# Performance work log

Hardware: AMD Instinct MI355X
Metric: run time of the kernel (lower is better)

## Reference

```python
import jax, jax.numpy as jnp
import numpy as np

N_V = 100000   # vertices
N_E = 20000    # hyperedges
N_PAIRS = 1600000  # incidence pairs
F = 128
H = 128
EPS = 1e-5


def setup_inputs() -> dict:
    key = jax.random.key(0)
    k1, k2, k3, k4 = jax.random.split(key, 4)
    X = jax.random.normal(k1, (N_V, F), dtype=jnp.float32)
    vertex_ids = jax.random.randint(k2, (N_PAIRS,), 0, N_V, dtype=jnp.int32)
    edge_ids = jax.random.randint(k3, (N_PAIRS,), 0, N_E, dtype=jnp.int32)
    W = jax.random.normal(k4, (F, H), dtype=jnp.float32) * (1.0 / np.sqrt(F))
    b = jnp.zeros((H,), dtype=jnp.float32)
    gamma = jnp.ones((H,), dtype=jnp.float32)
    beta = jnp.zeros((H,), dtype=jnp.float32)
    return {"X": X, "vertex_ids": vertex_ids, "edge_ids": edge_ids,
            "W": W, "b": b, "gamma": gamma, "beta": beta}


def _segment_mean(vals, ids, num_segments):
    s = jax.ops.segment_sum(vals, ids, num_segments=num_segments)
    cnt = jax.ops.segment_sum(jnp.ones((ids.shape[0], 1), vals.dtype), ids,
                              num_segments=num_segments)
    return s / jnp.maximum(cnt, 1.0)


def reference(X, vertex_ids, edge_ids, W, b, gamma, beta):
    # linear: theta
    h = X @ W + b                                    # [N_V, H]
    # batchnorm (batch statistics, as in training mode)
    mu = jnp.mean(h, axis=0)
    var = jnp.var(h, axis=0)
    h = (h - mu) * jax.lax.rsqrt(var + EPS) * gamma + beta
    # hypergraph v2v mean: vertex -> hyperedge mean, then hyperedge -> vertex mean
    Xe = _segment_mean(h[vertex_ids], edge_ids, N_E)   # [N_E, H]
    Xv = _segment_mean(Xe[edge_ids], vertex_ids, N_V)  # [N_V, H]
    # activation (ReLU); dropout is identity in eval
    return jax.nn.relu(Xv)
```

## Files before the change

kernel.cpp:

```cpp
#include <hip/hip_runtime.h>
#include <hip/hip_bf16.h>

#define N_V 100000
#define N_E 20000
#define N_P 1600000
#define FDIM 128
#define HDIM 128
#define BN_EPS 1e-5f

#define SORT_C 4096
#define SORT_BLOCKS ((N_P + SORT_C - 1) / SORT_C)
#define NB_E 313
#define EB_SHIFT 6
#define EB_REGION 9216
#define EB_SORT 5888
#define NB_V 391
#define VB_SHIFT 8
#define VB_REGION 8192
#define VB_SORT 4608
#define SENTINEL 0xFFFFFFFFu

#define EIDX_CAP 192
#define VIDX_CAP 64

typedef __attribute__((ext_vector_type(8))) short short8;
typedef __attribute__((ext_vector_type(4))) float floatx4;

__device__ __forceinline__ float bf_lo(unsigned u) {
    return __uint_as_float(u << 16);
}
__device__ __forceinline__ float bf_hi(unsigned u) {
    return __uint_as_float(u & 0xffff0000u);
}
__device__ __forceinline__ unsigned short f2bf(float f) {
    unsigned u = __float_as_uint(f);
    return (unsigned short)((u + 0x7fffu + ((u >> 16) & 1u)) >> 16);
}

__device__ __forceinline__ void acc4(float* s, const uint2& u) {
    s[0] += bf_lo(u.x); s[1] += bf_hi(u.x);
    s[2] += bf_lo(u.y); s[3] += bf_hi(u.y);
}

__device__ __forceinline__ void acc8(float* s, const uint4& u) {
    s[0] += bf_lo(u.x); s[1] += bf_hi(u.x);
    s[2] += bf_lo(u.y); s[3] += bf_hi(u.y);
    s[4] += bf_lo(u.z); s[5] += bf_hi(u.z);
    s[6] += bf_lo(u.w); s[7] += bf_hi(u.w);
}

#define GEMM_BLOCKS 625
#define WT_STRIDE 136
__global__ __launch_bounds__(256) void k_gemm_mfma(
    const float* __restrict__ X, const float* __restrict__ W,
    const float* __restrict__ bias, unsigned* __restrict__ h_u) {
    __shared__ unsigned short WTs[FDIM * WT_STRIDE];
    const int t = threadIdx.x;
    for (int idx = t; idx < FDIM * HDIM; idx += 256) {
        const int k = idx >> 7, m = idx & 127;
        WTs[m * WT_STRIDE + k] = f2bf(W[idx]);
    }
    __syncthreads();

    const int wave = t >> 6, lane = t & 63;
    const int quad = lane >> 4, sub = lane & 15;
    const int nstrips = N_V / 16;

    for (int s = blockIdx.x * 4 + wave; s < nstrips; s += GEMM_BLOCKS * 4) {
        const int row0 = s * 16;
        short8 xf[4];
        const float* xp = X + (size_t)(row0 + sub) * FDIM + quad * 8;
        #pragma unroll
        for (int kt = 0; kt < 4; ++kt) {
            const float4 a = *(const float4*)(xp + kt * 32);
            const float4 b2 = *(const float4*)(xp + kt * 32 + 4);
            short8 f;
            f[0] = (short)f2bf(a.x);  f[1] = (short)f2bf(a.y);
            f[2] = (short)f2bf(a.z);  f[3] = (short)f2bf(a.w);
            f[4] = (short)f2bf(b2.x); f[5] = (short)f2bf(b2.y);
            f[6] = (short)f2bf(b2.z); f[7] = (short)f2bf(b2.w);
            xf[kt] = f;
        }
        #pragma unroll
        for (int tile = 0; tile < 8; ++tile) {
            floatx4 acc = {0.f, 0.f, 0.f, 0.f};
            const unsigned short* wp =
                WTs + (tile * 16 + sub) * WT_STRIDE + quad * 8;
            #pragma unroll
            for (int kt = 0; kt < 4; ++kt) {
                const short8 af = *(const short8*)(wp + kt * 32);
                acc = __builtin_amdgcn_mfma_f32_16x16x32_bf16(af, xf[kt], acc,
                                                              0, 0, 0);
            }
            const int ch = tile * 16 + quad * 4;
            const float4 bb = *(const float4*)(bias + ch);
            const float c0 = acc[0] + bb.x, c1 = acc[1] + bb.y;
            const float c2 = acc[2] + bb.z, c3 = acc[3] + bb.w;
            const unsigned lo = (unsigned)f2bf(c0) | ((unsigned)f2bf(c1) << 16);
            const unsigned hi = (unsigned)f2bf(c2) | ((unsigned)f2bf(c3) << 16);
            uint2* dst = (uint2*)(h_u + (size_t)(row0 + sub) * 64 + (ch >> 1));
            *dst = make_uint2(lo, hi);
        }
    }
}

#define BN_BLOCKS 400
#define BN_RPB 250
__global__ __launch_bounds__(256) void k_bn_stats(
    const unsigned* __restrict__ h_u, float* __restrict__ sums ) {
    const int t = threadIdx.x;
    const int c8 = t & 15;
    const int rw = t >> 4;
    const int r0 = blockIdx.x * BN_RPB;
    const int r1 = min(r0 + BN_RPB, N_V);
    float s[8] = {0.f,0.f,0.f,0.f,0.f,0.f,0.f,0.f};
    float ss[8] = {0.f,0.f,0.f,0.f,0.f,0.f,0.f,0.f};
    for (int r = r0 + rw; r < r1; r += 16) {
        const uint4 u = *(const uint4*)(h_u + (size_t)r * 64 + c8 * 4);
        const float x0 = bf_lo(u.x), x1 = bf_hi(u.x);
        const float x2 = bf_lo(u.y), x3 = bf_hi(u.y);
        const float x4 = bf_lo(u.z), x5 = bf_hi(u.z);
        const float x6 = bf_lo(u.w), x7 = bf_hi(u.w);
        s[0]+=x0; ss[0]+=x0*x0;  s[1]+=x1; ss[1]+=x1*x1;
        s[2]+=x2; ss[2]+=x2*x2;  s[3]+=x3; ss[3]+=x3*x3;
        s[4]+=x4; ss[4]+=x4*x4;  s[5]+=x5; ss[5]+=x5*x5;
        s[6]+=x6; ss[6]+=x6*x6;  s[7]+=x7; ss[7]+=x7*x7;
    }
    #pragma unroll
    for (int k = 0; k < 8; ++k) {
        s[k]  += __shfl_xor(s[k], 16);  s[k]  += __shfl_xor(s[k], 32);
        ss[k] += __shfl_xor(ss[k], 16); ss[k] += __shfl_xor(ss[k], 32);
    }
    __shared__ float ls[128], lss[128];
    for (int k = t; k < 128; k += 256) { ls[k] = 0.f; lss[k] = 0.f; }
    __syncthreads();
    if ((t & 63) < 16) {
        #pragma unroll
        for (int k = 0; k < 8; ++k) {
            atomicAdd(&ls[c8 * 8 + k], s[k]);
            atomicAdd(&lss[c8 * 8 + k], ss[k]);
        }
    }
    __syncthreads();
    if (t < 128) {
        atomicAdd(&sums[t],       ls[t]);
        atomicAdd(&sums[128 + t], lss[t]);
    }
}

__global__ void k_bn_final(const float* __restrict__ sums,
                           const float* __restrict__ gamma,
                           const float* __restrict__ beta,
                           float* __restrict__ scale, float* __restrict__ shift) {
    const int c = threadIdx.x;
    const float inv_n = 1.0f / (float)N_V;
    const float mu  = sums[c] * inv_n;
    const float var = sums[128 + c] * inv_n - mu * mu;
    const float inv = rsqrtf(var + BN_EPS);
    const float sc  = gamma[c] * inv;
    scale[c] = sc;
    shift[c] = beta[c] - mu * sc;
}

__global__ __launch_bounds__(256) void k_sort_dual(
    const int* __restrict__ vid, const int* __restrict__ eid,
    int* __restrict__ gcntE, int* __restrict__ gcntV,
    unsigned* __restrict__ partE, unsigned* __restrict__ partV) {
    __shared__ unsigned stageE[SORT_C];
    __shared__ unsigned stageV[SORT_C];
    __shared__ int histE[NB_E], curE[NB_E], offsE[NB_E], gbaseE[NB_E];
    __shared__ int histV[NB_V], curV[NB_V], offsV[NB_V], gbaseV[NB_V];
    __shared__ int partial[256];
    const int t = threadIdx.x;
    const int p0 = blockIdx.x * SORT_C;
    const int n = min(SORT_C, N_P - p0);

    for (int k = t; k < NB_E; k += 256) histE[k] = 0;
    for (int k = t; k < NB_V; k += 256) histV[k] = 0;
    __syncthreads();
    for (int i = t; i < n; i += 256) {
        atomicAdd(&histE[((unsigned)eid[p0 + i]) >> EB_SHIFT], 1);
        atomicAdd(&histV[((unsigned)vid[p0 + i]) >> VB_SHIFT], 1);
    }
    __syncthreads();
    {
        constexpr int G = (NB_E + 255) / 256;
        int loc[G]; int s = 0;
        #pragma unroll
        for (int g = 0; g < G; ++g) {
            int idx = t * G + g; loc[g] = s;
            if (idx < NB_E) s += histE[idx];
        }
        partial[t] = s;
        __syncthreads();
        for (int d = 1; d < 256; d <<= 1) {
            int x = (t >= d) ? partial[t - d] : 0;
            __syncthreads(); partial[t] += x; __syncthreads();
        }
        const int base = t ? partial[t - 1] : 0;
        #pragma unroll
        for (int g = 0; g < G; ++g) {
            int idx = t * G + g;
            if (idx < NB_E) { offsE[idx] = base + loc[g]; curE[idx] = base + loc[g]; }
        }
        __syncthreads();
    }
    {
        constexpr int G = (NB_V + 255) / 256;
        int loc[G]; int s = 0;
        #pragma unroll
        for (int g = 0; g < G; ++g) {
            int idx = t * G + g; loc[g] = s;
            if (idx < NB_V) s += histV[idx];
        }
        partial[t] = s;
        __syncthreads();
        for (int d = 1; d < 256; d <<= 1) {
            int x = (t >= d) ? partial[t - d] : 0;
            __syncthreads(); partial[t] += x; __syncthreads();
        }
        const int base = t ? partial[t - 1] : 0;
        #pragma unroll
        for (int g = 0; g < G; ++g) {
            int idx = t * G + g;
            if (idx < NB_V) { offsV[idx] = base + loc[g]; curV[idx] = base + loc[g]; }
        }
        __syncthreads();
    }
    for (int i = t; i < n; i += 256) {
        const int ev = eid[p0 + i], vv = vid[p0 + i];
        const unsigned pkE = ((unsigned)(ev & 63) << 17) | (unsigned)vv;
        stageE[atomicAdd(&curE[(unsigned)ev >> EB_SHIFT], 1)] = pkE;
        const unsigned pkV = ((unsigned)(vv & 255) << 15) | (unsigned)ev;
        stageV[atomicAdd(&curV[(unsigned)vv >> VB_SHIFT], 1)] = pkV;
    }
    __syncthreads();
    for (int k = t; k < NB_E; k += 256) {
        const int c = histE[k];
        gbaseE[k] = c ? atomicAdd(&gcntE[k], (c + 15) & ~15) : 0;
    }
    for (int k = t; k < NB_V; k += 256) {
        const int c = histV[k];
        gbaseV[k] = c ? atomicAdd(&gcntV[k], (c + 15) & ~15) : 0;
    }
    __syncthreads();
    for (int k = t >> 3; k < NB_E; k += 32) {
        const int c = histE[k];
        if (c == 0) continue;
        int cpad = (c + 15) & ~15;
        const int gb = gbaseE[k];
        if (gb >= EB_REGION) continue;
        cpad = min(cpad, EB_REGION - gb);
        unsigned* dst = partE + (size_t)k * EB_REGION + gb;
        const int lo = offsE[k];
        for (int j = t & 7; j < cpad; j += 8)
            dst[j] = (j < c) ? stageE[lo + j] : SENTINEL;
    }
    for (int k = t >> 3; k < NB_V; k += 32) {
        const int c = histV[k];
        if (c == 0) continue;
        int cpad = (c + 15) & ~15;
        const int gb = gbaseV[k];
        if (gb >= VB_REGION) continue;
        cpad = min(cpad, VB_REGION - gb);
        unsigned* dst = partV + (size_t)k * VB_REGION + gb;
        const int lo = offsV[k];
        for (int j = t & 7; j < cpad; j += 8)
            dst[j] = (j < c) ? stageV[lo + j] : SENTINEL;
    }
}

template <int NKEY, int PACK_SHIFT, int CAP, int REGION, int STRIDE>
__global__ __launch_bounds__(256) void k_csr(
    const unsigned* __restrict__ part, const int* __restrict__ gcnt,
    int nkeys_total, int* __restrict__ segoff, int* __restrict__ segcnt,
    unsigned* __restrict__ csr) {
    __shared__ unsigned A[CAP];
    __shared__ unsigned B[CAP];
    __shared__ int hist[NKEY], offs[NKEY + 1], cur[NKEY];
    __shared__ int lcur;
    const int bkt = blockIdx.x;
    const int t = threadIdx.x;
    const int lane = t & 63;
    const unsigned mask = (1u << PACK_SHIFT) - 1u;
    const int tot = min(gcnt[bkt], REGION);
    const unsigned* src = part + (size_t)bkt * REGION;

    if (t == 0) lcur = 0;
    for (int k = t; k < NKEY; k += 256) hist[k] = 0;
    __syncthreads();
    for (int i = t; i < ((tot + 255) & ~255); i += 256) {
        unsigned a = (i < tot) ? src[i] : SENTINEL;
        const bool valid = (a != SENTINEL);
        const unsigned long long bal = __ballot(valid);
        int wbase = 0;
        if (lane == 0) wbase = atomicAdd(&lcur, __popcll(bal));
        wbase = __shfl(wbase, 0);
        if (valid) {
            const int pos = wbase + __popcll(bal & ((1ull << lane) - 1ull));
            if (pos < CAP) A[pos] = a;
        }
    }
    __syncthreads();
    const int total = min(lcur, CAP);
    for (int i = t; i < total; i += 256)
        atomicAdd(&hist[A[i] >> PACK_SHIFT], 1);
    __syncthreads();
    if (t == 0) {
        int acc = 0;
        for (int k = 0; k < NKEY; ++k) { offs[k] = acc; acc += hist[k]; }
        offs[NKEY] = acc;
    }
    for (int k = t; k < NKEY; k += 256) cur[k] = 0;
    __syncthreads();
    for (int i = t; i < total; i += 256) {
        const unsigned a = A[i];
        const int k = a >> PACK_SHIFT;
        const int pos = offs[k] + atomicAdd(&cur[k], 1);
        B[pos] = a & mask;
    }
    __syncthreads();
    unsigned* dst = csr + (size_t)bkt * STRIDE;
    for (int i = t; i < total; i += 256) dst[i] = B[i];
    for (int k = t; k < NKEY; k += 256) {
        const int g = bkt * NKEY + k;
        if (g < nkeys_total) {
            segoff[g] = bkt * STRIDE + offs[k];
            segcnt[g] = hist[k];
        }
    }
}

__global__ __launch_bounds__(256) void k_edge_gather(
    const unsigned* __restrict__ h_u, const unsigned* __restrict__ csrE,
    const int* __restrict__ eoff, const int* __restrict__ ecnt,
    const float* __restrict__ scale, const float* __restrict__ shift,
    unsigned* __restrict__ xe_u) {
    __shared__ int ib[4][EIDX_CAP];
    const int b = blockIdx.x;
    const int xcd = b & 7;
    const int half = xcd >> 2;
    const int grp = (b >> 3) * 4 + (xcd & 3);
    const int wave = threadIdx.x >> 6;
    const int e = grp * 4 + wave;
    const int l = threadIdx.x & 63;
    const int rg = l >> 4, c = l & 15;
    const int wbase = half * 32 + 2 * c;
    int o = 0, n = 0;
    if (e < N_E) { o = eoff[e]; n = ecnt[e]; }
    const int nc = min(n, EIDX_CAP);
    int* mi = ib[wave];
    for (int i = l; i < nc; i += 64) mi[i] = csrE[o + i];
    __syncthreads();

    float s[4] = {0.f, 0.f, 0.f, 0.f};
    int j = 0;
    for (; j + 31 < nc; j += 32) {
        const int r0 = mi[j + rg],      r1 = mi[j + 4 + rg];
        const int r2 = mi[j + 8 + rg],  r3 = mi[j + 12 + rg];
        const int r4 = mi[j + 16 + rg], r5 = mi[j + 20 + rg];
        const int r6 = mi[j + 24 + rg], r7 = mi[j + 28 + rg];
        const uint2 u0 = *(const uint2*)(h_u + (size_t)r0 * 64 + wbase);
        const uint2 u1 = *(const uint2*)(h_u + (size_t)r1 * 64 + wbase);
        const uint2 u2 = *(const uint2*)(h_u + (size_t)r2 * 64 + wbase);
        const uint2 u3 = *(const uint2*)(h_u + (size_t)r3 * 64 + wbase);
        const uint2 u4 = *(const uint2*)(h_u + (size_t)r4 * 64 + wbase);
        const uint2 u5 = *(const uint2*)(h_u + (size_t)r5 * 64 + wbase);
        const uint2 u6 = *(const uint2*)(h_u + (size_t)r6 * 64 + wbase);
        const uint2 u7 = *(const uint2*)(h_u + (size_t)r7 * 64 + wbase);
        acc4(s, u0); acc4(s, u1); acc4(s, u2); acc4(s, u3);
        acc4(s, u4); acc4(s, u5); acc4(s, u6); acc4(s, u7);
    }
    for (; j + 15 < nc; j += 16) {
        const int r0 = mi[j + rg],     r1 = mi[j + 4 + rg];
        const int r2 = mi[j + 8 + rg], r3 = mi[j + 12 + rg];
        const uint2 u0 = *(const uint2*)(h_u + (size_t)r0 * 64 + wbase);
        const uint2 u1 = *(const uint2*)(h_u + (size_t)r1 * 64 + wbase);
        const uint2 u2 = *(const uint2*)(h_u + (size_t)r2 * 64 + wbase);
        const uint2 u3 = *(const uint2*)(h_u + (size_t)r3 * 64 + wbase);
        acc4(s, u0); acc4(s, u1); acc4(s, u2); acc4(s, u3);
    }
    for (; j < nc; j += 4) {
        if (j + rg < nc) {
            const int r = mi[j + rg];
            const uint2 u = *(const uint2*)(h_u + (size_t)r * 64 + wbase);
            acc4(s, u);
        }
    }
    for (int jj = nc; jj < n; jj += 4) {
        if (jj + rg < n) {
            const int r = csrE[o + jj + rg];
            const uint2 u = *(const uint2*)(h_u + (size_t)r * 64 + wbase);
            acc4(s, u);
        }
    }
    #pragma unroll
    for (int k = 0; k < 4; ++k) {
        s[k] += __shfl_xor(s[k], 16);
        s[k] += __shfl_xor(s[k], 32);
    }
    if (e < N_E && rg == 0) {
        float m[4] = {0.f, 0.f, 0.f, 0.f};
        if (n > 0) {
            const float rc = 1.0f / (float)n;
            const float4 sc4 = ((const float4*)scale)[half * 16 + c];
            const float4 sh4 = ((const float4*)shift)[half * 16 + c];
            m[0] = sc4.x * s[0] * rc + sh4.x;
            m[1] = sc4.y * s[1] * rc + sh4.y;
            m[2] = sc4.z * s[2] * rc + sh4.z;
            m[3] = sc4.w * s[3] * rc + sh4.w;
        }
        uint2 pk;
        pk.x = (unsigned)f2bf(m[0]) | ((unsigned)f2bf(m[1]) << 16);
        pk.y = (unsigned)f2bf(m[2]) | ((unsigned)f2bf(m[3]) << 16);
        *(uint2*)(xe_u + (size_t)e * 64 + wbase) = pk;
    }
}

__global__ __launch_bounds__(256) void k_vert_gather(
    const unsigned* __restrict__ xe_u, const unsigned* __restrict__ csrV,
    const int* __restrict__ voff, const int* __restrict__ vcnt,
    float* __restrict__ out) {
    __shared__ int ib[4][VIDX_CAP];
    const int wave = threadIdx.x >> 6;
    const int v = blockIdx.x * 4 + wave;
    const int l = threadIdx.x & 63;
    const int g = l >> 4, c = l & 15;
    int o = 0, n = 0;
    if (v < N_V) { o = voff[v]; n = vcnt[v]; }
    const int nc = min(n, VIDX_CAP);
    int* mi = ib[wave];
    for (int i = l; i < nc; i += 64) mi[i] = csrV[o + i];
    __syncthreads();

    float s[8] = {0.f, 0.f, 0.f, 0.f, 0.f, 0.f, 0.f, 0.f};
    int j = 0;
    for (; j + 15 < nc; j += 16) {
        const int r0 = mi[j + g],     r1 = mi[j + 4 + g];
        const int r2 = mi[j + 8 + g], r3 = mi[j + 12 + g];
        const uint4 u0 = *(const uint4*)(xe_u + (size_t)r0 * 64 + 4 * c);
        const uint4 u1 = *(const uint4*)(xe_u + (size_t)r1 * 64 + 4 * c);
        const uint4 u2 = *(const uint4*)(xe_u + (size_t)r2 * 64 + 4 * c);
        const uint4 u3 = *(const uint4*)(xe_u + (size_t)r3 * 64 + 4 * c);
        acc8(s, u0); acc8(s, u1); acc8(s, u2); acc8(s, u3);
    }
    for (; j < nc; j += 4) {
        if (j + g < nc) {
            const int r = mi[j + g];
            const uint4 u = *(const uint4*)(xe_u + (size_t)r * 64 + 4 * c);
            acc8(s, u);
        }
    }
    for (int jj = nc; jj < n; jj += 4) {
        if (jj + g < n) {
            const int r = csrV[o + jj + g];
            const uint4 u = *(const uint4*)(xe_u + (size_t)r * 64 + 4 * c);
            acc8(s, u);
        }
    }
    #pragma unroll
    for (int k = 0; k < 8; ++k) {
        s[k] += __shfl_xor(s[k], 16);
        s[k] += __shfl_xor(s[k], 32);
    }
    if (v < N_V && g == 0) {
        const float rc = 1.0f / (float)max(n, 1);
        float4 r0, r1;
        r0.x = fmaxf(s[0] * rc, 0.f);
        r0.y = fmaxf(s[1] * rc, 0.f);
        r0.z = fmaxf(s[2] * rc, 0.f);
        r0.w = fmaxf(s[3] * rc, 0.f);
        r1.x = fmaxf(s[4] * rc, 0.f);
        r1.y = fmaxf(s[5] * rc, 0.f);
        r1.z = fmaxf(s[6] * rc, 0.f);
        r1.w = fmaxf(s[7] * rc, 0.f);
        ((float4*)out)[(size_t)v * 32 + 2 * c]     = r0;
        ((float4*)out)[(size_t)v * 32 + 2 * c + 1] = r1;
    }
}

extern "C" void kernel_launch(void* const* d_in, const int* in_sizes, int n_in,
                              void* d_out, int out_size, void* d_ws, size_t ws_size,
                              hipStream_t stream) {
    const float* X     = (const float*)d_in[0];
    const int*   vid   = (const int*)d_in[1];
    const int*   eid   = (const int*)d_in[2];
    const float* W     = (const float*)d_in[3];
    const float* b     = (const float*)d_in[4];
    const float* gamma = (const float*)d_in[5];
    const float* beta  = (const float*)d_in[6];
    float* out = (float*)d_out;

    char* ws = (char*)d_ws;
    unsigned* h_u   = (unsigned*)ws;  ws += (size_t)N_V * 64 * 4;
    unsigned* xe_u  = (unsigned*)ws;  ws += (size_t)N_E * 64 * 4;
    unsigned* partE = (unsigned*)ws;  ws += (size_t)NB_E * EB_REGION * 4;
    unsigned* partV = (unsigned*)ws;  ws += (size_t)NB_V * VB_REGION * 4;
    unsigned* csrE  = (unsigned*)ws;  ws += (size_t)NB_E * EB_SORT * 4;
    unsigned* csrV  = (unsigned*)ws;  ws += (size_t)NB_V * VB_SORT * 4;
    int* eoff = (int*)ws;             ws += (size_t)N_E * 4;
    int* ecnt = (int*)ws;             ws += (size_t)N_E * 4;
    int* voff = (int*)ws;             ws += (size_t)N_V * 4;
    int* vcnt = (int*)ws;             ws += (size_t)N_V * 4;
    char* zbase = ws;
    int*   gcntE = (int*)ws;          ws += (size_t)NB_E * 4;
    int*   gcntV = (int*)ws;          ws += (size_t)NB_V * 4;
    float* sums  = (float*)ws;        ws += 256 * 4;
    float* scale = (float*)ws;        ws += 128 * 4;
    float* shift = (float*)ws;        ws += 128 * 4;

    hipMemsetAsync(zbase, 0, (size_t)((char*)scale - zbase), stream);

    k_gemm_mfma<<<GEMM_BLOCKS, 256, 0, stream>>>(X, W, b, h_u);
    k_bn_stats<<<BN_BLOCKS, 256, 0, stream>>>(h_u, sums);
    k_bn_final<<<1, 128, 0, stream>>>(sums, gamma, beta, scale, shift);

    k_sort_dual<<<SORT_BLOCKS, 256, 0, stream>>>(vid, eid, gcntE, gcntV,
                                                 partE, partV);

    k_csr<64, 17, EB_SORT, EB_REGION, EB_SORT>
        <<<NB_E, 256, 0, stream>>>(partE, gcntE, N_E, eoff, ecnt, csrE);
    k_csr<256, 15, VB_SORT, VB_REGION, VB_SORT>
        <<<NB_V, 256, 0, stream>>>(partV, gcntV, N_V, voff, vcnt, csrV);

    k_edge_gather<<<(N_E / 4) * 2, 256, 0, stream>>>(h_u, csrE, eoff, ecnt,
                                                     scale, shift, xe_u);
    k_vert_gather<<<(N_V + 3) / 4, 256, 0, stream>>>(xe_u, csrV, voff, vcnt,
                                                     out);
}
```

Measured before the change: 310.6 us.

## Replace bucketed two-level sort with global-atomic histogram, scan, and scatter CSR build

The CSR construction used to be a per-block bucket sort into padded regions followed by per-bucket local counting sorts. It is now three simple kernels: a global-atomic histogram over every edge and vertex id, a single-pass scan per key set, and an atomic scatter straight into exact CSR arrays. This removes the padded intermediate buffers, the sentinel compaction and the capacity clamps. In exchange it relies on heavy global atomics and uncoalesced scattered writes, and the order of entries within each segment becomes nondeterministic.

Measured after the change: 778.1 us. 2.51x slower.

```diff
diff --git a/kernel.cpp b/kernel.cpp
--- a/kernel.cpp
+++ b/kernel.cpp
@@ -7,18 +7,6 @@
 #define FDIM 128
 #define HDIM 128
 #define BN_EPS 1e-5f
-
-#define SORT_C 4096
-#define SORT_BLOCKS ((N_P + SORT_C - 1) / SORT_C)
-#define NB_E 313
-#define EB_SHIFT 6
-#define EB_REGION 9216
-#define EB_SORT 5888
-#define NB_V 391
-#define VB_SHIFT 8
-#define VB_REGION 8192
-#define VB_SORT 4608
-#define SENTINEL 0xFFFFFFFFu
 
 #define EIDX_CAP 192
 #define VIDX_CAP 64
@@ -162,177 +150,70 @@
     shift[c] = beta[c] - mu * sc;
 }
 
-__global__ __launch_bounds__(256) void k_sort_dual(
+#define HIST_BLOCKS 1024
+__global__ __launch_bounds__(256) void k_hist(
     const int* __restrict__ vid, const int* __restrict__ eid,
-    int* __restrict__ gcntE, int* __restrict__ gcntV,
-    unsigned* __restrict__ partE, unsigned* __restrict__ partV) {
-    __shared__ unsigned stageE[SORT_C];
-    __shared__ unsigned stageV[SORT_C];
-    __shared__ int histE[NB_E], curE[NB_E], offsE[NB_E], gbaseE[NB_E];
-    __shared__ int histV[NB_V], curV[NB_V], offsV[NB_V], gbaseV[NB_V];
-    __shared__ int partial[256];
+    int* __restrict__ histE, int* __restrict__ histV) {
+    const int tid = blockIdx.x * 256 + threadIdx.x;
+    for (int i = tid; i < N_P / 4; i += HIST_BLOCKS * 256) {
+        const int4 e4 = ((const int4*)eid)[i];
+        const int4 v4 = ((const int4*)vid)[i];
+        atomicAdd(&histE[e4.x], 1); atomicAdd(&histE[e4.y], 1);
+        atomicAdd(&histE[e4.z], 1); atomicAdd(&histE[e4.w], 1);
+        atomicAdd(&histV[v4.x], 1); atomicAdd(&histV[v4.y], 1);
+        atomicAdd(&histV[v4.z], 1); atomicAdd(&histV[v4.w], 1);
+    }
+}
+
+__global__ __launch_bounds__(1024) void k_scan(
+    const int* __restrict__ histE, int* __restrict__ eoff, int* __restrict__ ecnt,
+    const int* __restrict__ histV, int* __restrict__ voff, int* __restrict__ vcnt) {
+    __shared__ int partial[1024];
     const int t = threadIdx.x;
-    const int p0 = blockIdx.x * SORT_C;
-    const int n = min(SORT_C, N_P - p0);
-
-    for (int k = t; k < NB_E; k += 256) histE[k] = 0;
-    for (int k = t; k < NB_V; k += 256) histV[k] = 0;
-    __syncthreads();
-    for (int i = t; i < n; i += 256) {
-        atomicAdd(&histE[((unsigned)eid[p0 + i]) >> EB_SHIFT], 1);
-        atomicAdd(&histV[((unsigned)vid[p0 + i]) >> VB_SHIFT], 1);
-    }
-    __syncthreads();
-    {
-        constexpr int G = (NB_E + 255) / 256;
-        int loc[G]; int s = 0;
-        #pragma unroll
-        for (int g = 0; g < G; ++g) {
-            int idx = t * G + g; loc[g] = s;
-            if (idx < NB_E) s += histE[idx];
-        }
-        partial[t] = s;
-        __syncthreads();
-        for (int d = 1; d < 256; d <<= 1) {
-            int x = (t >= d) ? partial[t - d] : 0;
-            __syncthreads(); partial[t] += x; __syncthreads();
-        }
-        const int base = t ? partial[t - 1] : 0;
-        #pragma unroll
-        for (int g = 0; g < G; ++g) {
-            int idx = t * G + g;
-            if (idx < NB_E) { offsE[idx] = base + loc[g]; curE[idx] = base + loc[g]; }
-        }
-        __syncthreads();
-    }
-    {
-        constexpr int G = (NB_V + 255) / 256;
-        int loc[G]; int s = 0;
-        #pragma unroll
-        for (int g = 0; g < G; ++g) {
-            int idx = t * G + g; loc[g] = s;
-            if (idx < NB_V) s += histV[idx];
-        }
-        partial[t] = s;
-        __syncthreads();
-        for (int d = 1; d < 256; d <<= 1) {
-            int x = (t >= d) ? partial[t - d] : 0;
-            __syncthreads(); partial[t] += x; __syncthreads();
-        }
-        const int base = t ? partial[t - 1] : 0;
-        #pragma unroll
-        for (int g = 0; g < G; ++g) {
-            int idx = t * G + g;
-            if (idx < NB_V) { offsV[idx] = base + loc[g]; curV[idx] = base + loc[g]; }
-        }
-        __syncthreads();
-    }
-    for (int i = t; i < n; i += 256) {
-        const int ev = eid[p0 + i], vv = vid[p0 + i];
-        const unsigned pkE = ((unsigned)(ev & 63) << 17) | (unsigned)vv;
-        stageE[atomicAdd(&curE[(unsigned)ev >> EB_SHIFT], 1)] = pkE;
-        const unsigned pkV = ((unsigned)(vv & 255) << 15) | (unsigned)ev;
-        stageV[atomicAdd(&curV[(unsigned)vv >> VB_SHIFT], 1)] = pkV;
-    }
-    __syncthreads();
-    for (int k = t; k < NB_E; k += 256) {
-        const int c = histE[k];
-        gbaseE[k] = c ? atomicAdd(&gcntE[k], (c + 15) & ~15) : 0;
-    }
-    for (int k = t; k < NB_V; k += 256) {
-        const int c = histV[k];
-        gbaseV[k] = c ? atomicAdd(&gcntV[k], (c + 15) & ~15) : 0;
-    }
-    __syncthreads();
-    for (int k = t >> 3; k < NB_E; k += 32) {
-        const int c = histE[k];
-        if (c == 0) continue;
-        int cpad = (c + 15) & ~15;
-        const int gb = gbaseE[k];
-        if (gb >= EB_REGION) continue;
-        cpad = min(cpad, EB_REGION - gb);
-        unsigned* dst = partE + (size_t)k * EB_REGION + gb;
-        const int lo = offsE[k];
-        for (int j = t & 7; j < cpad; j += 8)
-            dst[j] = (j < c) ? stageE[lo + j] : SENTINEL;
-    }
-    for (int k = t >> 3; k < NB_V; k += 32) {
-        const int c = histV[k];
-        if (c == 0) continue;
-        int cpad = (c + 15) & ~15;
-        const int gb = gbaseV[k];
-        if (gb >= VB_REGION) continue;
-        cpad = min(cpad, VB_REGION - gb);
-        unsigned* dst = partV + (size_t)k * VB_REGION + gb;
-        const int lo = offsV[k];
-        for (int j = t & 7; j < cpad; j += 8)
-            dst[j] = (j < c) ? stageV[lo + j] : SENTINEL;
-    }
-}
-
-template <int NKEY, int PACK_SHIFT, int CAP, int REGION, int STRIDE>
-__global__ __launch_bounds__(256) void k_csr(
-    const unsigned* __restrict__ part, const int* __restrict__ gcnt,
-    int nkeys_total, int* __restrict__ segoff, int* __restrict__ segcnt,
-    unsigned* __restrict__ csr) {
-    __shared__ unsigned A[CAP];
-    __shared__ unsigned B[CAP];
-    __shared__ int hist[NKEY], offs[NKEY + 1], cur[NKEY];
-    __shared__ int lcur;
-    const int bkt = blockIdx.x;
-    const int t = threadIdx.x;
-    const int lane = t & 63;
-    const unsigned mask = (1u << PACK_SHIFT) - 1u;
-    const int tot = min(gcnt[bkt], REGION);
-    const unsigned* src = part + (size_t)bkt * REGION;
-
-    if (t == 0) lcur = 0;
-    for (int k = t; k < NKEY; k += 256) hist[k] = 0;
-    __syncthreads();
-    for (int i = t; i < ((tot + 255) & ~255); i += 256) {
-        unsigned a = (i < tot) ? src[i] : SENTINEL;
-        const bool valid = (a != SENTINEL);
-        const unsigned long long bal = __ballot(valid);
-        int wbase = 0;
-        if (lane == 0) wbase = atomicAdd(&lcur, __popcll(bal));
-        wbase = __shfl(wbase, 0);
-        if (valid) {
-            const int pos = wbase + __popcll(bal & ((1ull << lane) - 1ull));
-            if (pos < CAP) A[pos] = a;
-        }
-    }
-    __syncthreads();
-    const int total = min(lcur, CAP);
-    for (int i = t; i < total; i += 256)
-        atomicAdd(&hist[A[i] >> PACK_SHIFT], 1);
-    __syncthreads();
-    if (t == 0) {
-        int acc = 0;
-        for (int k = 0; k < NKEY; ++k) { offs[k] = acc; acc += hist[k]; }
-        offs[NKEY] = acc;
-    }
-    for (int k = t; k < NKEY; k += 256) cur[k] = 0;
-    __syncthreads();
-    for (int i = t; i < total; i += 256) {
-        const unsigned a = A[i];
-        const int k = a >> PACK_SHIFT;
-        const int pos = offs[k] + atomicAdd(&cur[k], 1);
-        B[pos] = a & mask;
-    }
-    __syncthreads();
-    unsigned* dst = csr + (size_t)bkt * STRIDE;
-    for (int i = t; i < total; i += 256) dst[i] = B[i];
-    for (int k = t; k < NKEY; k += 256) {
-        const int g = bkt * NKEY + k;
-        if (g < nkeys_total) {
-            segoff[g] = bkt * STRIDE + offs[k];
-            segcnt[g] = hist[k];
-        }
+    const int* hist; int* off; int* cnt; int n;
+    if (blockIdx.x == 0) { hist = histE; off = eoff; cnt = ecnt; n = N_E; }
+    else                 { hist = histV; off = voff; cnt = vcnt; n = N_V; }
+    const int chunk = (n + 1023) / 1024;
+    const int lo = t * chunk, hi = min(lo + chunk, n);
+    int s = 0;
+    for (int i = lo; i < hi; ++i) s += hist[i];
+    partial[t] = s;
+    __syncthreads();
+    for (int d = 1; d < 1024; d <<= 1) {
+        int x = (t >= d) ? partial[t - d] : 0;
+        __syncthreads(); partial[t] += x; __syncthreads();
+    }
+    int base = t ? partial[t - 1] : 0;
+    for (int i = lo; i < hi; ++i) {
+        const int h = hist[i];
+        off[i] = base; cnt[i] = h; base += h;
+    }
+}
+
+#define SCAT_BLOCKS 1024
+__global__ __launch_bounds__(256) void k_scatter(
+    const int* __restrict__ vid, const int* __restrict__ eid,
+    const int* __restrict__ eoff, const int* __restrict__ voff,
+    int* __restrict__ curE, int* __restrict__ curV,
+    int* __restrict__ csrE, int* __restrict__ csrV) {
+    const int tid = blockIdx.x * 256 + threadIdx.x;
+    for (int i = tid; i < N_P / 4; i += SCAT_BLOCKS * 256) {
+        const int4 e4 = ((const int4*)eid)[i];
+        const int4 v4 = ((const int4*)vid)[i];
+        int p;
+        p = atomicAdd(&curE[e4.x], 1); csrE[eoff[e4.x] + p] = v4.x;
+        p = atomicAdd(&curE[e4.y], 1); csrE[eoff[e4.y] + p] = v4.y;
+        p = atomicAdd(&curE[e4.z], 1); csrE[eoff[e4.z] + p] = v4.z;
+        p = atomicAdd(&curE[e4.w], 1); csrE[eoff[e4.w] + p] = v4.w;
+        p = atomicAdd(&curV[v4.x], 1); csrV[voff[v4.x] + p] = e4.x;
+        p = atomicAdd(&curV[v4.y], 1); csrV[voff[v4.y] + p] = e4.y;
+        p = atomicAdd(&curV[v4.z], 1); csrV[voff[v4.z] + p] = e4.z;
+        p = atomicAdd(&curV[v4.w], 1); csrV[voff[v4.w] + p] = e4.w;
     }
 }
 
 __global__ __launch_bounds__(256) void k_edge_gather(
-    const unsigned* __restrict__ h_u, const unsigned* __restrict__ csrE,
+    const unsigned* __restrict__ h_u, const int* __restrict__ csrE,
     const int* __restrict__ eoff, const int* __restrict__ ecnt,
     const float* __restrict__ scale, const float* __restrict__ shift,
     unsigned* __restrict__ xe_u) {
@@ -418,7 +299,7 @@
 }
 
 __global__ __launch_bounds__(256) void k_vert_gather(
-    const unsigned* __restrict__ xe_u, const unsigned* __restrict__ csrV,
+    const unsigned* __restrict__ xe_u, const int* __restrict__ csrV,
     const int* __restrict__ voff, const int* __restrict__ vcnt,
     float* __restrict__ out) {
     __shared__ int ib[4][VIDX_CAP];
@@ -494,17 +375,17 @@
     char* ws = (char*)d_ws;
     unsigned* h_u   = (unsigned*)ws;  ws += (size_t)N_V * 64 * 4;
     unsigned* xe_u  = (unsigned*)ws;  ws += (size_t)N_E * 64 * 4;
-    unsigned* partE = (unsigned*)ws;  ws += (size_t)NB_E * EB_REGION * 4;
-    unsigned* partV = (unsigned*)ws;  ws += (size_t)NB_V * VB_REGION * 4;
-    unsigned* csrE  = (unsigned*)ws;  ws += (size_t)NB_E * EB_SORT * 4;
-    unsigned* csrV  = (unsigned*)ws;  ws += (size_t)NB_V * VB_SORT * 4;
+    int* csrE = (int*)ws;             ws += (size_t)N_P * 4;
+    int* csrV = (int*)ws;             ws += (size_t)N_P * 4;
     int* eoff = (int*)ws;             ws += (size_t)N_E * 4;
     int* ecnt = (int*)ws;             ws += (size_t)N_E * 4;
     int* voff = (int*)ws;             ws += (size_t)N_V * 4;
     int* vcnt = (int*)ws;             ws += (size_t)N_V * 4;
     char* zbase = ws;
-    int*   gcntE = (int*)ws;          ws += (size_t)NB_E * 4;
-    int*   gcntV = (int*)ws;          ws += (size_t)NB_V * 4;
+    int*   histE = (int*)ws;          ws += (size_t)N_E * 4;
+    int*   histV = (int*)ws;          ws += (size_t)N_V * 4;
+    int*   curE  = (int*)ws;          ws += (size_t)N_E * 4;
+    int*   curV  = (int*)ws;          ws += (size_t)N_V * 4;
     float* sums  = (float*)ws;        ws += 256 * 4;
     float* scale = (float*)ws;        ws += 128 * 4;
     float* shift = (float*)ws;        ws += 128 * 4;
@@ -515,13 +396,10 @@
     k_bn_stats<<<BN_BLOCKS, 256, 0, stream>>>(h_u, sums);
     k_bn_final<<<1, 128, 0, stream>>>(sums, gamma, beta, scale, shift);
 
-    k_sort_dual<<<SORT_BLOCKS, 256, 0, stream>>>(vid, eid, gcntE, gcntV,
-                                                 partE, partV);
-
-    k_csr<64, 17, EB_SORT, EB_REGION, EB_SORT>
-        <<<NB_E, 256, 0, stream>>>(partE, gcntE, N_E, eoff, ecnt, csrE);
-    k_csr<256, 15, VB_SORT, VB_REGION, VB_SORT>
-        <<<NB_V, 256, 0, stream>>>(partV, gcntV, N_V, voff, vcnt, csrV);
+    k_hist<<<HIST_BLOCKS, 256, 0, stream>>>(vid, eid, histE, histV);
+    k_scan<<<2, 1024, 0, stream>>>(histE, eoff, ecnt, histV, voff, vcnt);
+    k_scatter<<<SCAT_BLOCKS, 256, 0, stream>>>(vid, eid, eoff, voff,
+                                               curE, curV, csrE, csrV);
 
     k_edge_gather<<<(N_E / 4) * 2, 256, 0, stream>>>(h_u, csrE, eoff, ecnt,
                                                      scale, shift, xe_u);
```
